# Kernel tuning notes

Hardware: AMD Instinct MI355X
Metric: run time of the kernel (lower is better)

Reference implementation:

```python
import jax, jax.numpy as jnp
import numpy as np

DT = 0.2
T = 30
SIZE_TAB = [10, 1024, 1024, 784]
BATCH = 256

def rho(x):
    # hard-sigmoid nonlinearity used throughout the EP/SNN codebase
    return jnp.clip(x, 0.0, 1.0)

def setup_inputs() -> dict:
    key = jax.random.key(0)
    ks = jax.random.split(key, 8)
    data = jax.random.uniform(ks[0], (BATCH, SIZE_TAB[3]), dtype=jnp.float32)
    s0 = jnp.zeros((BATCH, SIZE_TAB[0]), jnp.float32)
    s1 = jnp.zeros((BATCH, SIZE_TAB[1]), jnp.float32)
    s2 = jnp.zeros((BATCH, SIZE_TAB[2]), jnp.float32)
    def lin(k, out_d, in_d):
        bound = 1.0 / np.sqrt(in_d)
        return jax.random.uniform(k, (out_d, in_d), jnp.float32, -bound, bound)
    # w0: size_tab[1]->size_tab[0] (bias), w1 = w0.T (no bias)
    W0 = lin(ks[1], SIZE_TAB[0], SIZE_TAB[1]); b0 = jnp.zeros((SIZE_TAB[0],), jnp.float32)
    W1 = W0.T  # transpose init, faithful to __init__
    # w2: size_tab[2]->size_tab[1] (bias), w3 = w2.T (no bias)
    W2 = lin(ks[2], SIZE_TAB[1], SIZE_TAB[2]); b2 = jnp.zeros((SIZE_TAB[1],), jnp.float32)
    W3 = W2.T
    # w4 (= w[-1]): size_tab[3]->size_tab[2], default bias
    W4 = lin(ks[3], SIZE_TAB[2], SIZE_TAB[3]); b4 = jnp.zeros((SIZE_TAB[2],), jnp.float32)
    return {"data": data, "s0": s0, "s1": s1, "s2": s2,
            "W0": W0, "b0": b0, "W1": W1, "W2": W2, "b2": b2,
            "W3": W3, "W4": W4, "b4": b4}

def reference(data, s0, s1, s2, W0, b0, W1, W2, b2, W3, W4, b4):
    # Free phase (beta=0): T Euler steps of the leaky-integrator SNN.
    base = jax.random.key(42)
    def step(carry, t):
        s0, s1, s2 = carry
        k = jax.random.fold_in(base, t)
        k0, k1, k2 = jax.random.split(k, 3)
        # bernoulli spikes: rand < rho(s)
        sp0 = (jax.random.uniform(k0, s0.shape) < rho(s0)).astype(s0.dtype)
        sp1 = (jax.random.uniform(k1, s1.shape) < rho(s1)).astype(s1.dtype)
        sp2 = (jax.random.uniform(k2, s2.shape) < rho(s2)).astype(s2.dtype)
        # dsdt computed from pre-update states (as in torch)
        ds0 = -s0 + sp1 @ W0.T + b0
        ds1 = -s1 + sp2 @ W2.T + b2 + sp0 @ W1.T
        ds2 = -s2 + data @ W4.T + b4 + rho(s1) @ W3.T  # last layer uses s (not spikes) from data layer
        n0 = jnp.clip(s0 + DT * ds0, 0.0, 1.0)
        n1 = jnp.clip(s1 + DT * ds1, 0.0, 1.0)
        n2 = jnp.clip(s2 + DT * ds2, 0.0, 1.0)
        return (n0, n1, n2), None
    (s0, s1, s2), _ = jax.lax.scan(step, (s0, s1, s2), jnp.arange(T))
    return s0, s1, s2, data  # s[-1] (data layer) is never updated
```

## Files before the change

kernel.cpp:

```cpp
#include <hip/hip_runtime.h>
#include <stdint.h>

#define DTv 0.2f

typedef __attribute__((ext_vector_type(8))) short short8;
typedef __attribute__((ext_vector_type(4))) float f32x4;
#define MFMA16(A,B,C) __builtin_amdgcn_mfma_f32_16x16x32_bf16(A,B,C,0,0,0)
#define GLOAD16(gp, lp) __builtin_amdgcn_global_load_lds( \
    (const __attribute__((address_space(1))) void*)(gp), \
    (__attribute__((address_space(3))) void*)(lp), 16, 0, 0)

__device__ __forceinline__ uint32_t rotl32(uint32_t v, uint32_t r){ return (v<<r)|(v>>(32u-r)); }

__device__ __forceinline__ void tf2x32(uint32_t k0, uint32_t k1, uint32_t& x0, uint32_t& x1){
  const uint32_t k2 = k0 ^ k1 ^ 0x1BD11BDAu;
  x0 += k0; x1 += k1;
#define RND(r) { x0 += x1; x1 = rotl32(x1,(r)); x1 ^= x0; }
  RND(13u) RND(15u) RND(26u) RND(6u)
  x0 += k1; x1 += k2 + 1u;
  RND(17u) RND(29u) RND(16u) RND(24u)
  x0 += k2; x1 += k0 + 2u;
  RND(13u) RND(15u) RND(26u) RND(6u)
  x0 += k0; x1 += k1 + 3u;
  RND(17u) RND(29u) RND(16u) RND(24u)
  x0 += k1; x1 += k2 + 4u;
  RND(13u) RND(15u) RND(26u) RND(6u)
  x0 += k2; x1 += k0 + 5u;
#undef RND
}

__device__ __forceinline__ float u01(uint32_t bits){
  return __uint_as_float((bits >> 9) | 0x3f800000u) - 1.0f;
}

__device__ __forceinline__ void step_keys(int t, uint32_t* K){
  uint32_t c0 = 0u, c1 = (uint32_t)t;
  tf2x32(0u, 42u, c0, c1);
#pragma unroll
  for (int i = 0; i < 3; ++i){
    uint32_t a = 0u, b = (uint32_t)i;
    tf2x32(c0, c1, a, b);
    K[2*i] = a; K[2*i+1] = b;
  }
}

__device__ __forceinline__ ushort f2bf(float f){
  uint32_t u = __float_as_uint(f);
  u += 0x7fffu + ((u >> 16) & 1u);
  return (ushort)(u >> 16);
}
__device__ __forceinline__ float bf2f(ushort h){ return __uint_as_float(((uint32_t)h) << 16); }

__global__ __launch_bounds__(256) void d2p_kernel(
    const float* __restrict__ data, const float* __restrict__ W4, float* __restrict__ Pd2)
{
  __shared__ float As[16][64];
  __shared__ float Bs[16][64];
  const int tb = blockIdx.x / 7;
  const int ch = blockIdx.x % 7;
  const int kb = ch * 112;
  const int R0 = (tb >> 4) << 6;
  const int C0 = (tb & 15) << 6;
  const int tid = threadIdx.x;
  const int ty = tid >> 4, tx = tid & 15;
  const int mA = tid >> 2, kqA = (tid & 3) << 2;
  float acc[4][4] = {{0.f}};
  for (int kk = 0; kk < 112; kk += 16){
    const float4 a = *(const float4*)&data[(R0+mA)*784 + kb + kk + kqA];
    As[kqA+0][mA]=a.x; As[kqA+1][mA]=a.y; As[kqA+2][mA]=a.z; As[kqA+3][mA]=a.w;
    const float4 b = *(const float4*)&W4[(C0+mA)*784 + kb + kk + kqA];
    Bs[kqA+0][mA]=b.x; Bs[kqA+1][mA]=b.y; Bs[kqA+2][mA]=b.z; Bs[kqA+3][mA]=b.w;
    __syncthreads();
#pragma unroll
    for (int k=0;k<16;k++){
      const float4 av = *(const float4*)&As[k][ty<<2];
      const float4 bv = *(const float4*)&Bs[k][tx<<2];
      acc[0][0]=fmaf(av.x,bv.x,acc[0][0]); acc[0][1]=fmaf(av.x,bv.y,acc[0][1]);
      acc[0][2]=fmaf(av.x,bv.z,acc[0][2]); acc[0][3]=fmaf(av.x,bv.w,acc[0][3]);
      acc[1][0]=fmaf(av.y,bv.x,acc[1][0]); acc[1][1]=fmaf(av.y,bv.y,acc[1][1]);
      acc[1][2]=fmaf(av.y,bv.z,acc[1][2]); acc[1][3]=fmaf(av.y,bv.w,acc[1][3]);
      acc[2][0]=fmaf(av.z,bv.x,acc[2][0]); acc[2][1]=fmaf(av.z,bv.y,acc[2][1]);
      acc[2][2]=fmaf(av.z,bv.z,acc[2][2]); acc[2][3]=fmaf(av.z,bv.w,acc[2][3]);
      acc[3][0]=fmaf(av.w,bv.x,acc[3][0]); acc[3][1]=fmaf(av.w,bv.y,acc[3][1]);
      acc[3][2]=fmaf(av.w,bv.z,acc[3][2]); acc[3][3]=fmaf(av.w,bv.w,acc[3][3]);
    }
    __syncthreads();
  }
  float* P = Pd2 + ch*262144;
#pragma unroll
  for (int i=0;i<4;i++){
    const int r = R0 + (ty<<2) + i;
    float4 o; float* op=(float*)&o;
#pragma unroll
    for (int j=0;j<4;j++) op[j] = acc[i][j];
    *(float4*)&P[r*1024 + C0 + (tx<<2)] = o;
  }
}

__global__ __launch_bounds__(256) void d2r_kernel(
    const float* __restrict__ Pd2, const float* __restrict__ b4, float* __restrict__ D2)
{
  const int e = (blockIdx.x*256 + threadIdx.x) << 2;
  float4 acc = *(const float4*)&Pd2[e];
#pragma unroll
  for (int p = 1; p < 7; ++p){
    const float4 q = *(const float4*)&Pd2[p*262144 + e];
    acc.x += q.x; acc.y += q.y; acc.z += q.z; acc.w += q.w;
  }
  const float4 bb = *(const float4*)&b4[e & 1023];
  acc.x += bb.x; acc.y += bb.y; acc.z += bb.z; acc.w += bb.w;
  *(float4*)&D2[e] = acc;
}

__device__ __forceinline__ void arrive(unsigned* xbar, unsigned* cnt, int grp, unsigned a){
  const unsigned old = __hip_atomic_fetch_add(&xbar[grp << 5], 1u,
                        __ATOMIC_RELEASE, __HIP_MEMORY_SCOPE_AGENT);
  if (old == a*32u + 31u)
    __hip_atomic_fetch_add(cnt, 1u, __ATOMIC_RELEASE, __HIP_MEMORY_SCOPE_AGENT);
}
__device__ __forceinline__ void spinwait(unsigned* cnt, unsigned target){
  unsigned it = 0;
  while (__hip_atomic_load(cnt, __ATOMIC_RELAXED, __HIP_MEMORY_SCOPE_AGENT) < target){
    __builtin_amdgcn_s_sleep(2);
    if (++it > (1u<<26)) break;
  }
  __builtin_amdgcn_fence(__ATOMIC_ACQUIRE, "agent");
}

__global__ __launch_bounds__(512) void persist_kernel(
    const float* __restrict__ data, const float* __restrict__ s0i,
    const float* __restrict__ s1i, const float* __restrict__ s2i,
    const float* __restrict__ W1g, const float* __restrict__ W2,
    const float* __restrict__ W3, const float* __restrict__ b0g,
    const float* __restrict__ b2g, const float* __restrict__ D2,
    float* __restrict__ sp0A, float* __restrict__ sp0B,
    unsigned* __restrict__ sp1bA, unsigned* __restrict__ sp1bB,
    unsigned* __restrict__ sp2bA, unsigned* __restrict__ sp2bB,
    ushort* __restrict__ ahA, ushort* __restrict__ ahB,
    ushort* __restrict__ alA, ushort* __restrict__ alB,
    float* __restrict__ out, unsigned* __restrict__ bar)
{
  extern __shared__ char lds[];
  short* Bh   = (short*)lds;
  short* Bl   = (short*)(lds + 32768);
  short* Abuf = (short*)(lds + 65536);
  float* Sst  = (float*)(lds + 131072);
  float* AUX  = (float*)(lds + 139264);
  float* MISC = (float*)(lds + 147456);
  uint32_t* K  = (uint32_t*)MISC;
  float* b0s   = MISC + 8;
  float* s0st  = MISC + 18;
  float* s0red = MISC + 38;
  float* b2s   = MISC + 120;
  float* W1epi = MISC + 136;

  unsigned* xbar = bar;
  unsigned* cA   = bar + 256;
  unsigned* cB   = bar + 320;

  const int bid = blockIdx.x, tid = threadIdx.x;
  const int grp = bid & 7;
  const int g2 = (bid >> 2) & 1, sub = (bid >> 1) & 1;
  const int coltile = ((bid & 1) << 5) + (bid >> 3);
  const int cb = coltile << 4;
  const int w = tid >> 6, lane = tid & 63, lr = lane & 15, sl = lane >> 4;
  const int r0s = ((coltile << 1) + sub) << 1;

  {
    const float* Wsrc = g2 ? W3 : W2;
    const int row = tid >> 5, seg = tid & 31;
    const float* src = &Wsrc[(cb + row)*1024 + seg*32];
#pragma unroll
    for (int g = 0; g < 4; ++g){
      short8 h8, l8;
#pragma unroll
      for (int j = 0; j < 8; ++j){
        const float f = src[g*8 + j];
        const ushort hh = f2bf(f);
        h8[j] = (short)hh;
        l8[j] = (short)f2bf(f - bf2f(hh));
      }
      const int kg = seg*4 + g;
      *(short8*)&Bh[(kg<<7) + (row<<3)] = h8;
      *(short8*)&Bl[(kg<<7) + (row<<3)] = l8;
    }
  }
  for (int i = tid; i < 160; i += 512) W1epi[i] = W1g[(cb + i/10)*10 + (i%10)];
  float w1c[20];
#pragma unroll
  for (int j = 0; j < 10; ++j){
    w1c[j]      = W1g[tid*10 + j];
    w1c[10 + j] = W1g[(tid + 512)*10 + j];
  }
  {
    const float* Ssrc = g2 ? s2i : s1i;
    for (int idx = tid; idx < 2048; idx += 512){
      const int r = idx >> 4, c = idx & 15;
      Sst[idx] = Ssrc[(((sub<<7)+r)<<10) + cb + c];
    }
    if (g2){
      for (int idx = tid; idx < 2048; idx += 512){
        const int r = idx >> 4, c = idx & 15;
        AUX[idx] = D2[(((sub<<7)+r)<<10) + cb + c];
      }
    }
  }
  if (tid < 10) b0s[tid] = b0g[tid];
  if (g2 && tid < 20) s0st[tid] = s0i[(r0s + tid/10)*10 + (tid%10)];
  if (tid < 16) b2s[tid] = b2g[cb + tid];
  for (int idx = tid; idx < 784; idx += 512)
    out[526848 + bid*784 + idx] = data[bid*784 + idx];
  if (tid == 0) step_keys(0, K);
  __syncthreads();

  {
    const uint32_t kk0 = g2 ? K[4] : K[2];
    const uint32_t kk1 = g2 ? K[5] : K[3];
    ushort* sp1u = (ushort*)sp1bA;
    ushort* sp2u = (ushort*)sp2bA;
#pragma unroll
    for (int i2 = 0; i2 < 4; ++i2){
      const int rloc = (w<<4) + (sl<<2) + i2;
      const int R = (sub<<7) + rloc;
      const int e = (R << 10) + cb + lr;
      const float v = fminf(fmaxf(Sst[(rloc<<4) + lr], 0.f), 1.f);
      uint32_t x0 = 0u, x1 = (uint32_t)e;
      tf2x32(kk0, kk1, x0, x1);
      const bool sp = (u01(x0 ^ x1) < v);
      const unsigned long long bt = __ballot(sp ? 1 : 0);
      if (!g2){
        const ushort hh = f2bf(v);
        ahA[e] = hh; alA[e] = f2bf(v - bf2f(hh));
        if (lr == 0) sp1u[R*64 + (cb>>4)] = (ushort)((bt >> (sl<<4)) & 0xFFFFu);
      } else {
        if (lr == 0) sp2u[R*64 + (cb>>4)] = (ushort)((bt >> (sl<<4)) & 0xFFFFu);
      }
    }
    if (g2 && tid < 20){
      const float v = fminf(fmaxf(s0st[tid], 0.f), 1.f);
      const int e = (r0s + tid/10)*10 + (tid%10);
      uint32_t x0 = 0u, x1 = (uint32_t)e;
      tf2x32(K[0], K[1], x0, x1);
      sp0A[e] = (u01(x0 ^ x1) < v) ? 1.0f : 0.0f;
    }
  }
  __syncthreads();
  if (tid == 0) arrive(xbar, g2 ? cB : cA, grp, 0u);

  const int r0g = (sub << 7) + (w << 4);
  const int gbase = ((r0g + (lane >> 2)) << 10) + ((((lane & 3) ^ ((lane >> 2) & 3))) << 3);
  const int fragoff = (lr << 5) + ((sl ^ (lr & 3)) << 3);
  const int shl = sl << 3;
  short* AW = Abuf + (w << 12);

#pragma unroll 1
  for (int t = 0; t < 30; ++t){
    const int cur = t & 1;
    const float*    sp0c  = cur ? sp0B  : sp0A;   float*    sp0n  = cur ? sp0A  : sp0B;
    const unsigned* sp1bc = cur ? sp1bB : sp1bA;  unsigned* sp1bn = cur ? sp1bA : sp1bB;
    const unsigned* sp2bc = cur ? sp2bB : sp2bA;  unsigned* sp2bn = cur ? sp2bA : sp2bB;
    const ushort*   ahc   = cur ? ahB   : ahA;    ushort*   ahn   = cur ? ahA   : ahB;
    const ushort*   alc   = cur ? alB   : alA;    ushort*   aln   = cur ? alA   : alB;

    if (tid == 0){
      step_keys(t+1, K);
      spinwait(g2 ? cA : cB, 4u*(t+1));
    }
    __syncthreads();

    if (!g2){
      for (int idx = tid; idx < 1280; idx += 512) AUX[idx] = sp0c[sub*1280 + idx];
      __syncthreads();
    } else {
#pragma unroll 1
      for (int rr = 0; rr < 2; ++rr){
        const int r = r0s + rr;
        const unsigned* mrow = sp1bc + r*32;
        const unsigned d0 = mrow[tid >> 5];
        const unsigned d1 = mrow[16 + (tid >> 5)];
        const float sv0 = (float)((d0 >> (tid & 31)) & 1u);
        const float sv1 = (float)((d1 >> (tid & 31)) & 1u);
        float a0_[10];
#pragma unroll
        for (int c2 = 0; c2 < 10; ++c2){
          float a = fmaf(sv0, w1c[c2], 0.f);
          a0_[c2] = fmaf(sv1, w1c[10 + c2], a);
        }
#pragma unroll
        for (int c2 = 0; c2 < 10; ++c2){
          float v = a0_[c2];
          v += __shfl_xor(v, 1);  v += __shfl_xor(v, 2);  v += __shfl_xor(v, 4);
          v += __shfl_xor(v, 8);  v += __shfl_xor(v, 16); v += __shfl_xor(v, 32);
          a0_[c2] = v;
        }
        if (lane == 0){
#pragma unroll
          for (int c2 = 0; c2 < 10; ++c2) s0red[w*10 + c2] = a0_[c2];
        }
        __syncthreads();
        if (tid < 10){
          float sum = 0.f;
#pragma unroll
          for (int ww = 0; ww < 8; ++ww) sum += s0red[ww*10 + tid];
          const float s = s0st[rr*10 + tid];
          float nv = s + DTv*(-s + sum + b0s[tid]);
          nv = fminf(fmaxf(nv, 0.f), 1.f);
          s0st[rr*10 + tid] = nv;
          const int e = r*10 + tid;
          uint32_t x0 = 0u, x1 = (uint32_t)e;
          tf2x32(K[0], K[1], x0, x1);
          sp0n[e] = (u01(x0 ^ x1) < nv) ? 1.0f : 0.0f;
        }
        __syncthreads();
      }
    }

    f32x4 acc0 = {0.f,0.f,0.f,0.f}, acc1 = {0.f,0.f,0.f,0.f}, acc2 = {0.f,0.f,0.f,0.f};
    if (!g2){
      const unsigned* mrow = sp2bc + (r0g + lr)*32;
      const uint4 m0 = *(const uint4*)(mrow +  0);
      const uint4 m1 = *(const uint4*)(mrow +  4);
      const uint4 m2 = *(const uint4*)(mrow +  8);
      const uint4 m3 = *(const uint4*)(mrow + 12);
      const uint4 m4 = *(const uint4*)(mrow + 16);
      const uint4 m5 = *(const uint4*)(mrow + 20);
      const uint4 m6 = *(const uint4*)(mrow + 24);
      const uint4 m7 = *(const uint4*)(mrow + 28);
#define U0(ks, DW) { \
      const unsigned b_ = ((DW) >> shl) & 0xFFu; \
      short8 a8; \
      a8[0]=(short)(((b_    )&1)?0x3F80:0); a8[1]=(short)(((b_>>1)&1)?0x3F80:0); \
      a8[2]=(short)(((b_>>2)&1)?0x3F80:0); a8[3]=(short)(((b_>>3)&1)?0x3F80:0); \
      a8[4]=(short)(((b_>>4)&1)?0x3F80:0); a8[5]=(short)(((b_>>5)&1)?0x3F80:0); \
      a8[6]=(short)(((b_>>6)&1)?0x3F80:0); a8[7]=(short)(((b_>>7)&1)?0x3F80:0); \
      const int ib = ((((ks)<<2)+sl)<<7) + (lr<<3); \
      const short8 bh8 = *(const short8*)(Bh + ib); \
      const short8 bl8 = *(const short8*)(Bl + ib); \
      acc0 = MFMA16(a8, bh8, acc0); \
      acc1 = MFMA16(a8, bl8, acc1); }
      U0(0,m0.x)  U0(1,m0.y)  U0(2,m0.z)  U0(3,m0.w)
      U0(4,m1.x)  U0(5,m1.y)  U0(6,m1.z)  U0(7,m1.w)
      U0(8,m2.x)  U0(9,m2.y)  U0(10,m2.z) U0(11,m2.w)
      U0(12,m3.x) U0(13,m3.y) U0(14,m3.z) U0(15,m3.w)
      U0(16,m4.x) U0(17,m4.y) U0(18,m4.z) U0(19,m4.w)
      U0(20,m5.x) U0(21,m5.y) U0(22,m5.z) U0(23,m5.w)
      U0(24,m6.x) U0(25,m6.y) U0(26,m6.z) U0(27,m6.w)
      U0(28,m7.x) U0(29,m7.y) U0(30,m7.z) U0(31,m7.w)
#undef U0
    } else {
      const short* Ah0 = (const short*)ahc + gbase;
      const short* Al0 = (const short*)alc + gbase;
#define G1_ISSUE(c) { GLOAD16(Ah0 + ((c)<<5), AW + (((c)&3)<<10)); \
                      GLOAD16(Al0 + ((c)<<5), AW + (((c)&3)<<10) + 512); }
#define G1_ITER(c, vm) { \
      asm volatile("s_waitcnt vmcnt(" #vm ")" ::: "memory"); \
      __builtin_amdgcn_sched_barrier(0); \
      const short8 h8  = *(const short8*)(AW + (((c)&3)<<10) + fragoff); \
      const short8 l8  = *(const short8*)(AW + (((c)&3)<<10) + 512 + fragoff); \
      const int ib = ((((c)<<2)+sl)<<7) + (lr<<3); \
      const short8 bh8 = *(const short8*)(Bh + ib); \
      const short8 bl8 = *(const short8*)(Bl + ib); \
      acc0 = MFMA16(h8, bh8, acc0); \
      acc1 = MFMA16(h8, bl8, acc1); \
      acc2 = MFMA16(l8, bh8, acc2); \
      __builtin_amdgcn_sched_barrier(0); \
      if ((c) < 28) G1_ISSUE((c)+4) }
      G1_ISSUE(0) G1_ISSUE(1) G1_ISSUE(2) G1_ISSUE(3)
      G1_ITER(0,6)  G1_ITER(1,6)  G1_ITER(2,6)  G1_ITER(3,6)
      G1_ITER(4,6)  G1_ITER(5,6)  G1_ITER(6,6)  G1_ITER(7,6)
      G1_ITER(8,6)  G1_ITER(9,6)  G1_ITER(10,6) G1_ITER(11,6)
      G1_ITER(12,6) G1_ITER(13,6) G1_ITER(14,6) G1_ITER(15,6)
      G1_ITER(16,6) G1_ITER(17,6) G1_ITER(18,6) G1_ITER(19,6)
      G1_ITER(20,6) G1_ITER(21,6) G1_ITER(22,6) G1_ITER(23,6)
      G1_ITER(24,6) G1_ITER(25,6) G1_ITER(26,6) G1_ITER(27,6)
      G1_ITER(28,6) G1_ITER(29,4) G1_ITER(30,2) G1_ITER(31,0)
#undef G1_ITER
#undef G1_ISSUE
    }

    {
      const bool emit = (t < 29);
      if (!g2){
        const uint32_t kk0 = K[2], kk1 = K[3];
        ushort* sp1u = (ushort*)sp1bn;
#pragma unroll
        for (int i2 = 0; i2 < 4; ++i2){
          const int rloc = (w<<4) + (sl<<2) + i2;
          float v = acc0[i2] + acc1[i2];
          float sm = 0.f;
#pragma unroll
          for (int k2 = 0; k2 < 10; ++k2)
            sm = fmaf(AUX[rloc*10 + k2], W1epi[lr*10 + k2], sm);
          v += b2s[lr] + sm;
          const float s = Sst[(rloc<<4) + lr];
          float nv = s + DTv*(-s + v);
          nv = fminf(fmaxf(nv, 0.f), 1.f);
          Sst[(rloc<<4) + lr] = nv;
          if (emit){
            const int R = (sub<<7) + rloc;
            const int e = (R << 10) + cb + lr;
            uint32_t x0 = 0u, x1 = (uint32_t)e;
            tf2x32(kk0, kk1, x0, x1);
            const bool sp = (u01(x0 ^ x1) < nv);
            const ushort hh = f2bf(nv);
            ahn[e] = hh; aln[e] = f2bf(nv - bf2f(hh));
            const unsigned long long bt = __ballot(sp ? 1 : 0);
            if (lr == 0) sp1u[R*64 + (cb>>4)] = (ushort)((bt >> (sl<<4)) & 0xFFFFu);
          }
        }
      } else {
        const uint32_t kk0 = K[4], kk1 = K[5];
        ushort* sp2u = (ushort*)sp2bn;
#pragma unroll
        for (int i2 = 0; i2 < 4; ++i2){
          const int rloc = (w<<4) + (sl<<2) + i2;
          float v = acc0[i2] + acc1[i2] + acc2[i2];
          v += AUX[(rloc<<4) + lr];
          const float s = Sst[(rloc<<4) + lr];
          float nv = s + DTv*(-s + v);
          nv = fminf(fmaxf(nv, 0.f), 1.f);
          Sst[(rloc<<4) + lr] = nv;
          if (emit){
            const int R = (sub<<7) + rloc;
            const int e = (R << 10) + cb + lr;
            uint32_t x0 = 0u, x1 = (uint32_t)e;
            tf2x32(kk0, kk1, x0, x1);
            const bool sp = (u01(x0 ^ x1) < nv);
            const unsigned long long bt = __ballot(sp ? 1 : 0);
            if (lr == 0) sp2u[R*64 + (cb>>4)] = (ushort)((bt >> (sl<<4)) & 0xFFFFu);
          }
        }
      }
    }

    __syncthreads();
    if (tid == 0 && t < 29) arrive(xbar, g2 ? cB : cA, grp, (unsigned)(t+1));
  }

  __syncthreads();
  for (int idx = tid; idx < 2048; idx += 512){
    const int r = (sub<<7) + (idx >> 4);
    const int c = cb + (idx & 15);
    out[(g2 ? 264704 : 2560) + (r << 10) + c] = Sst[idx];
  }
  if (g2 && tid < 20) out[(r0s + tid/10)*10 + (tid%10)] = s0st[tid];
}

extern "C" void kernel_launch(void* const* d_in, const int* in_sizes, int n_in,
                              void* d_out, int out_size, void* d_ws, size_t ws_size,
                              hipStream_t stream)
{
  const float* data = (const float*)d_in[0];
  const float* s0i  = (const float*)d_in[1];
  const float* s1i  = (const float*)d_in[2];
  const float* s2i  = (const float*)d_in[3];
  const float* b0   = (const float*)d_in[5];
  const float* W1   = (const float*)d_in[6];
  const float* W2   = (const float*)d_in[7];
  const float* b2   = (const float*)d_in[8];
  const float* W3   = (const float*)d_in[9];
  const float* W4   = (const float*)d_in[10];
  const float* b4   = (const float*)d_in[11];
  float* out = (float*)d_out;
  float* ws  = (float*)d_ws;

  float* sp0A = ws + 0;
  float* sp0B = ws + 2560;
  float* D2   = ws + 5120;
  float* Pd2  = ws + 267264;
  ushort* ahA = (ushort*)(ws + 2102272);
  ushort* ahB = (ushort*)(ws + 2233344);
  ushort* alA = (ushort*)(ws + 2364416);
  ushort* alB = (ushort*)(ws + 2495488);
  unsigned* sp1bA = (unsigned*)(ws + 2626560);
  unsigned* sp1bB = (unsigned*)(ws + 2634752);
  unsigned* sp2bA = (unsigned*)(ws + 2642944);
  unsigned* sp2bB = (unsigned*)(ws + 2651136);
  unsigned* bar   = (unsigned*)(ws + 2659328);

  hipMemsetAsync(bar, 0, 2048, stream);
  d2p_kernel<<<448,256,0,stream>>>(data, W4, Pd2);
  d2r_kernel<<<256,256,0,stream>>>(Pd2, b4, D2);
  persist_kernel<<<256,512,149504,stream>>>(
      data, s0i, s1i, s2i, W1, W2, W3, b0, b2, D2,
      sp0A, sp0B, sp1bA, sp1bB, sp2bA, sp2bB,
      ahA, ahB, alA, alB, out, bar);
}
```

Measured before the change: 517.1 us.

## Use system-coherent stores and relaxed atomics for grid barrier publishing

Cross-block state stores (spike bitmasks, bf16 hi/lo activations, sp0) now use inline asm with sc0 sc1 bits, so they write through the caches. Each block then waits on vmcnt(0) before its barrier arrive, and the arrive atomics drop from release to relaxed ordering. The aim is to avoid the heavy L2 writeback or invalidate that a release fence at agent scope triggers on every step. Paired bf16 halves are also packed through a lane shuffle into 32-bit stores, which halves the store count. The risk is memory-ordering correctness, which now depends on the cache bits and the explicit waitcnt rather than on compiler-placed fences.

```diff
diff --git a/kernel.cpp b/kernel.cpp
--- a/kernel.cpp
+++ b/kernel.cpp
@@ -9,6 +9,16 @@
 #define GLOAD16(gp, lp) __builtin_amdgcn_global_load_lds( \
     (const __attribute__((address_space(1))) void*)(gp), \
     (__attribute__((address_space(3))) void*)(lp), 16, 0, 0)
+
+__device__ __forceinline__ void st_u16_sc(ushort* p, uint v){
+  asm volatile("global_store_short %0, %1, off sc0 sc1" :: "v"(p), "v"(v) : "memory");
+}
+__device__ __forceinline__ void st_u32_sc(uint* p, uint v){
+  asm volatile("global_store_dword %0, %1, off sc0 sc1" :: "v"(p), "v"(v) : "memory");
+}
+__device__ __forceinline__ void st_f32_sc(float* p, float v){
+  asm volatile("global_store_dword %0, %1, off sc0 sc1" :: "v"(p), "v"(v) : "memory");
+}
 
 __device__ __forceinline__ uint32_t rotl32(uint32_t v, uint32_t r){ return (v<<r)|(v>>(32u-r)); }
 
@@ -114,9 +124,9 @@
 
 __device__ __forceinline__ void arrive(unsigned* xbar, unsigned* cnt, int grp, unsigned a){
   const unsigned old = __hip_atomic_fetch_add(&xbar[grp << 5], 1u,
-                        __ATOMIC_RELEASE, __HIP_MEMORY_SCOPE_AGENT);
+                        __ATOMIC_RELAXED, __HIP_MEMORY_SCOPE_AGENT);
   if (old == a*32u + 31u)
-    __hip_atomic_fetch_add(cnt, 1u, __ATOMIC_RELEASE, __HIP_MEMORY_SCOPE_AGENT);
+    __hip_atomic_fetch_add(cnt, 1u, __ATOMIC_RELAXED, __HIP_MEMORY_SCOPE_AGENT);
 }
 __device__ __forceinline__ void spinwait(unsigned* cnt, unsigned target){
   unsigned it = 0;
@@ -229,11 +239,17 @@
       const bool sp = (u01(x0 ^ x1) < v);
       const unsigned long long bt = __ballot(sp ? 1 : 0);
       if (!g2){
-        const ushort hh = f2bf(v);
-        ahA[e] = hh; alA[e] = f2bf(v - bf2f(hh));
-        if (lr == 0) sp1u[R*64 + (cb>>4)] = (ushort)((bt >> (sl<<4)) & 0xFFFFu);
+        const int hh = (int)f2bf(v);
+        const int ll = (int)f2bf(v - bf2f((ushort)hh));
+        const int hp = __shfl_down(hh, 1);
+        const int lp = __shfl_down(ll, 1);
+        if (!(lr & 1)){
+          st_u32_sc((uint*)&ahA[e], (uint)(ushort)hh | ((uint)(ushort)hp << 16));
+          st_u32_sc((uint*)&alA[e], (uint)(ushort)ll | ((uint)(ushort)lp << 16));
+        }
+        if (lr == 0) st_u16_sc(&sp1u[R*64 + (cb>>4)], (uint)((bt >> (sl<<4)) & 0xFFFFu));
       } else {
-        if (lr == 0) sp2u[R*64 + (cb>>4)] = (ushort)((bt >> (sl<<4)) & 0xFFFFu);
+        if (lr == 0) st_u16_sc(&sp2u[R*64 + (cb>>4)], (uint)((bt >> (sl<<4)) & 0xFFFFu));
       }
     }
     if (g2 && tid < 20){
@@ -241,9 +257,10 @@
       const int e = (r0s + tid/10)*10 + (tid%10);
       uint32_t x0 = 0u, x1 = (uint32_t)e;
       tf2x32(K[0], K[1], x0, x1);
-      sp0A[e] = (u01(x0 ^ x1) < v) ? 1.0f : 0.0f;
-    }
-  }
+      st_f32_sc(&sp0A[e], (u01(x0 ^ x1) < v) ? 1.0f : 0.0f);
+    }
+  }
+  asm volatile("s_waitcnt vmcnt(0)" ::: "memory");
   __syncthreads();
   if (tid == 0) arrive(xbar, g2 ? cB : cA, grp, 0u);
 
@@ -309,7 +326,7 @@
           const int e = r*10 + tid;
           uint32_t x0 = 0u, x1 = (uint32_t)e;
           tf2x32(K[0], K[1], x0, x1);
-          sp0n[e] = (u01(x0 ^ x1) < nv) ? 1.0f : 0.0f;
+          st_f32_sc(&sp0n[e], (u01(x0 ^ x1) < nv) ? 1.0f : 0.0f);
         }
         __syncthreads();
       }
@@ -402,10 +419,16 @@
             uint32_t x0 = 0u, x1 = (uint32_t)e;
             tf2x32(kk0, kk1, x0, x1);
             const bool sp = (u01(x0 ^ x1) < nv);
-            const ushort hh = f2bf(nv);
-            ahn[e] = hh; aln[e] = f2bf(nv - bf2f(hh));
+            const int hh = (int)f2bf(nv);
+            const int ll = (int)f2bf(nv - bf2f((ushort)hh));
+            const int hp = __shfl_down(hh, 1);
+            const int lp = __shfl_down(ll, 1);
+            if (!(lr & 1)){
+              st_u32_sc((uint*)&ahn[e], (uint)(ushort)hh | ((uint)(ushort)hp << 16));
+              st_u32_sc((uint*)&aln[e], (uint)(ushort)ll | ((uint)(ushort)lp << 16));
+            }
             const unsigned long long bt = __ballot(sp ? 1 : 0);
-            if (lr == 0) sp1u[R*64 + (cb>>4)] = (ushort)((bt >> (sl<<4)) & 0xFFFFu);
+            if (lr == 0) st_u16_sc(&sp1u[R*64 + (cb>>4)], (uint)((bt >> (sl<<4)) & 0xFFFFu));
           }
         }
       } else {
@@ -427,12 +450,13 @@
             tf2x32(kk0, kk1, x0, x1);
             const bool sp = (u01(x0 ^ x1) < nv);
             const unsigned long long bt = __ballot(sp ? 1 : 0);
-            if (lr == 0) sp2u[R*64 + (cb>>4)] = (ushort)((bt >> (sl<<4)) & 0xFFFFu);
+            if (lr == 0) st_u16_sc(&sp2u[R*64 + (cb>>4)], (uint)((bt >> (sl<<4)) & 0xFFFFu));
           }
         }
       }
     }
 
+    asm volatile("s_waitcnt vmcnt(0)" ::: "memory");
     __syncthreads();
     if (tid == 0 && t < 29) arrive(xbar, g2 ? cB : cA, grp, (unsigned)(t+1));
   }
```

New measurement: 455.4 us. 1.14x faster.
